# Performance work log

Measured on AMD Instinct MI355X. Metric: run time of the kernel, lower is better.

Reference implementation:

```python
import jax, jax.numpy as jnp
import numpy as np


def setup_inputs() -> dict:
    key = jax.random.key(0)
    ks = jax.random.split(key, 7)
    N, D, H1, H2, M = 16384, 2048, 512, 32, 2048
    return {
        "x": jax.random.normal(ks[0], (N, D), dtype=jnp.float32),
        "W1": jax.random.normal(ks[1], (H1, D), dtype=jnp.float32) * (1.0 / np.sqrt(D)),
        "b1": jax.random.normal(ks[2], (H1,), dtype=jnp.float32) * 0.01,
        "W2": jax.random.normal(ks[3], (H2, H1), dtype=jnp.float32) * (1.0 / np.sqrt(H1)),
        "b2": jax.random.normal(ks[4], (H2,), dtype=jnp.float32) * 0.01,
        "a_memory": jax.random.normal(ks[5], (M, H2), dtype=jnp.float32),
        "n_memory": jax.random.normal(ks[6], (M, H2), dtype=jnp.float32),
    }


def reference(x, W1, b1, W2, b2, a_memory, n_memory):
    # MLP per forward(): linear -> relu -> (dropout p=0) -> linear -> (dropout p=0)
    h = jax.nn.relu(x @ W1.T + b1)          # [N, 512]
    feat = h @ W2.T + b2                     # [N, 32] (no ReLU in forward path)
    inv_d = 1.0 / feat.shape[1]
    # caption_score(mem, f) = max_j mean(mem_j * f) = max_j (mem_j . f) / 32
    a_score = jnp.max(feat @ a_memory.T, axis=1) * inv_d  # [N]
    n_score = jnp.max(feat @ n_memory.T, axis=1) * inv_d  # [N]
    return jax.nn.sigmoid(a_score - n_score)
```

## Files before the change

### kernel.cpp

```cpp
#include <hip/hip_runtime.h>
#include <hip/hip_bf16.h>

typedef __attribute__((ext_vector_type(8))) __bf16 bf16x8;
typedef __attribute__((ext_vector_type(4))) float f32x4;

#define NROWS 16384
#define DIM   2048
#define NH1   512
#define NH2   32
#define MMEM  2048
#define BK    32
#define NT    (DIM / BK)

#define W1O ((size_t)0)
#define W2O ((size_t)2097152)
#define AMO ((size_t)2129920)
#define NMO ((size_t)2260992)
#define HO  ((size_t)2392064)

__device__ __forceinline__ f32x4 mfma16(bf16x8 a, bf16x8 b, f32x4 c) {
    return __builtin_amdgcn_mfma_f32_16x16x32_bf16(a, b, c, 0, 0, 0);
}

__device__ __forceinline__ void gload_lds16(const void* g, void* l) {
    __builtin_amdgcn_global_load_lds(
        (const __attribute__((address_space(1))) void*)g,
        (__attribute__((address_space(3))) void*)l, 16, 0, 0);
}

__device__ __forceinline__ bf16x8 cvt8(f32x4 a, f32x4 b) {
    bf16x8 o;
    o[0] = (__bf16)a[0]; o[1] = (__bf16)a[1]; o[2] = (__bf16)a[2]; o[3] = (__bf16)a[3];
    o[4] = (__bf16)b[0]; o[5] = (__bf16)b[1]; o[6] = (__bf16)b[2]; o[7] = (__bf16)b[3];
    return o;
}

struct bf4 { __bf16 a, b, c, d; };

__global__ void cvt_all_kernel(const float* __restrict__ w1f, __bf16* __restrict__ w1b,
                               const float* __restrict__ w2f, __bf16* __restrict__ w2b,
                               const float* __restrict__ amf, __bf16* __restrict__ amb,
                               const float* __restrict__ nmf, __bf16* __restrict__ nmb) {
    const int g = blockIdx.x * blockDim.x + threadIdx.x;
    const int T = gridDim.x * blockDim.x;
    for (int i = g; i < (NH1 * DIM) / 4; i += T) {
        const float4 v = *reinterpret_cast<const float4*>(w1f + i * 4);
        *reinterpret_cast<bf4*>(w1b + i * 4) = { (__bf16)v.x, (__bf16)v.y, (__bf16)v.z, (__bf16)v.w };
    }
    for (int i = g; i < (NH2 * NH1) / 4; i += T) {
        const float4 v = *reinterpret_cast<const float4*>(w2f + i * 4);
        *reinterpret_cast<bf4*>(w2b + i * 4) = { (__bf16)v.x, (__bf16)v.y, (__bf16)v.z, (__bf16)v.w };
    }
    for (int i = g; i < (MMEM * NH2) / 4; i += T) {
        const float4 v = *reinterpret_cast<const float4*>(amf + i * 4);
        *reinterpret_cast<bf4*>(amb + i * 4) = { (__bf16)v.x, (__bf16)v.y, (__bf16)v.z, (__bf16)v.w };
    }
    for (int i = g; i < (MMEM * NH2) / 4; i += T) {
        const float4 v = *reinterpret_cast<const float4*>(nmf + i * 4);
        *reinterpret_cast<bf4*>(nmb + i * 4) = { (__bf16)v.x, (__bf16)v.y, (__bf16)v.z, (__bf16)v.w };
    }
}

__global__ __launch_bounds__(256, 2) void gemm1_kernel(
    const float*  __restrict__ Xf,
    const __bf16* __restrict__ W1,
    const float*  __restrict__ b1,
    __bf16* __restrict__ Hout)
{
    __shared__ float  As[3][128 * BK];
    __shared__ __bf16 Bs[3][128 * BK];
    const int tid  = threadIdx.x;
    const int lane = tid & 63;
    const int wave = tid >> 6;
    const int b = blockIdx.x;
    const int orig = (b & 7) * 64 + (b >> 3);
    const int bn = orig & 3;
    const int bm = orig >> 2;
    const size_t brow = (size_t)bm * 128;
    const int bcol = bn * 128;
    const int wr = wave >> 1, wc = wave & 1;

    f32x4 acc[4][4];
#pragma unroll
    for (int m = 0; m < 4; ++m)
#pragma unroll
        for (int n = 0; n < 4; ++n) acc[m][n] = (f32x4){0.f, 0.f, 0.f, 0.f};

    const int aRowT = tid >> 3;
    const int cA    = (tid & 7) ^ (aRowT & 7);
    const float* aSrcBase = Xf + (brow + aRowT) * (size_t)DIM + cA * 4;
    const int bl  = (tid & 7) ^ ((tid >> 3) & 7);
    const int bh  = bl >> 2;
    const int bc  = bl & 3;
    const __bf16* bSrcBase = W1 + (size_t)(bcol + 2 * (tid >> 3) + bh) * DIM + bc * 8;

#define STAGE(T, BI)                                                          \
    {                                                                         \
        const int k0_ = (T) * BK;                                             \
        _Pragma("unroll")                                                     \
        for (int q = 0; q < 4; ++q)                                           \
            gload_lds16(aSrcBase + (size_t)q * 32 * DIM + k0_,                \
                        (char*)As[BI] + q * 4096 + tid * 16);                 \
        _Pragma("unroll")                                                     \
        for (int q = 0; q < 2; ++q)                                           \
            gload_lds16(bSrcBase + (size_t)q * 64 * DIM + k0_,                \
                        (char*)Bs[BI] + q * 4096 + tid * 16);                 \
    }

    const int l15 = lane & 15;
    const int kc  = lane >> 4;
    const int l7  = lane & 7;
    const int rABase = wr * 64 + l15;
    const int aSlot0 = ((2 * kc)     ^ l7) << 4;
    const int aSlot1 = ((2 * kc + 1) ^ l7) << 4;
    const int bByteBase = (wc * 32 + (l15 >> 1)) * 128 +
                          ((((l15 & 1) * 4 + kc) ^ (l15 >> 1)) << 4);

#define COMPUTE(BI)                                                           \
    {                                                                         \
        const char* Ac = (const char*)As[BI];                                 \
        const char* Bc = (const char*)Bs[BI];                                 \
        bf16x8 av[4], bv[4];                                                  \
        _Pragma("unroll")                                                     \
        for (int m = 0; m < 4; ++m) {                                         \
            const int rowB = (rABase + m * 16) * 128;                         \
            f32x4 lo = *(const f32x4*)(Ac + rowB + aSlot0);                   \
            f32x4 hi = *(const f32x4*)(Ac + rowB + aSlot1);                   \
            av[m] = cvt8(lo, hi);                                             \
        }                                                                     \
        _Pragma("unroll")                                                     \
        for (int n = 0; n < 4; ++n)                                           \
            bv[n] = *(const bf16x8*)(Bc + bByteBase + n * 1024);              \
        __builtin_amdgcn_s_setprio(1);                                        \
        _Pragma("unroll")                                                     \
        for (int m = 0; m < 4; ++m)                                           \
            _Pragma("unroll")                                                 \
            for (int n = 0; n < 4; ++n)                                       \
                acc[m][n] = mfma16(av[m], bv[n], acc[m][n]);                  \
        __builtin_amdgcn_s_setprio(0);                                        \
    }

    STAGE(0, 0);
    STAGE(1, 1);

    for (int t = 0; t < NT - 2; ++t) {
        const int bi = t % 3;
        asm volatile("s_waitcnt vmcnt(6)" ::: "memory");
        __builtin_amdgcn_s_barrier();
        __builtin_amdgcn_sched_barrier(0);
        COMPUTE(bi);
        __builtin_amdgcn_sched_barrier(0);
        const int bnx = (t + 2) % 3;
        STAGE(t + 2, bnx);
    }
    {
        asm volatile("s_waitcnt vmcnt(6)" ::: "memory");
        __builtin_amdgcn_s_barrier();
        __builtin_amdgcn_sched_barrier(0);
        COMPUTE((NT - 2) % 3);
        asm volatile("s_waitcnt vmcnt(0)" ::: "memory");
        __builtin_amdgcn_s_barrier();
        __builtin_amdgcn_sched_barrier(0);
        COMPUTE((NT - 1) % 3);
    }
#undef STAGE
#undef COMPUTE

#pragma unroll
    for (int n = 0; n < 4; ++n) {
        const int gcol = bcol + wc * 64 + n * 16 + l15;
        const float bias = b1[gcol];
#pragma unroll
        for (int m = 0; m < 4; ++m) {
            const size_t grow0 = brow + wr * 64 + m * 16 + kc * 4;
#pragma unroll
            for (int r = 0; r < 4; ++r) {
                float v = acc[m][n][r] + bias;
                v = v > 0.f ? v : 0.f;
                Hout[(grow0 + r) * NH1 + gcol] = (__bf16)v;
            }
        }
    }
}

__global__ __launch_bounds__(512) void tail_kernel(
    const __bf16* __restrict__ Hin,
    const __bf16* __restrict__ W2b,
    const float*  __restrict__ b2,
    const __bf16* __restrict__ Am,
    const __bf16* __restrict__ Nm,
    float* __restrict__ out)
{
    __shared__ __bf16 featLds[64 * 32];
    __shared__ float aMaxLds[2][64];
    __shared__ float nMaxLds[2][64];
    const int tid  = threadIdx.x;
    const int lane = tid & 63;
    const int wave = tid >> 6;
    const int rowBase = blockIdx.x * 64;
    const int l15 = lane & 15;
    const int kc  = lane >> 4;
    const int rgrp  = (wave & 3) * 16;
    const int jHalf = wave >> 2;

    if (wave < 4) {
        f32x4 acc0 = {0.f,0.f,0.f,0.f}, acc1 = {0.f,0.f,0.f,0.f};
        const size_t hrow = (size_t)(rowBase + rgrp + l15) * NH1;
#pragma unroll
        for (int kk = 0; kk < 16; ++kk) {
            bf16x8 a  = *(const bf16x8*)(Hin + hrow + kk * 32 + kc * 8);
            bf16x8 w0 = *(const bf16x8*)(W2b + (size_t)l15 * NH1 + kk * 32 + kc * 8);
            bf16x8 w1 = *(const bf16x8*)(W2b + (size_t)(16 + l15) * NH1 + kk * 32 + kc * 8);
            acc0 = mfma16(a, w0, acc0);
            acc1 = mfma16(a, w1, acc1);
        }
        const float bias0 = b2[l15], bias1 = b2[16 + l15];
#pragma unroll
        for (int r = 0; r < 4; ++r) {
            const int lr = rgrp + kc * 4 + r;
            featLds[lr * 32 + l15]      = (__bf16)(acc0[r] + bias0);
            featLds[lr * 32 + 16 + l15] = (__bf16)(acc1[r] + bias1);
        }
    }
    __syncthreads();

    const bf16x8 af = *(const bf16x8*)&featLds[(rgrp + l15) * 32 + kc * 8];

    float rmaxA[4], rmaxN[4];
#pragma unroll
    for (int r = 0; r < 4; ++r) { rmaxA[r] = -1e30f; rmaxN[r] = -1e30f; }
    const f32x4 zero = {0.f,0.f,0.f,0.f};
    const int jBase = jHalf * (MMEM / 2);
#pragma unroll 2
    for (int jt = 0; jt < (MMEM / 2) / 16; jt += 4) {
        bf16x8 ba[4], bb[4];
#pragma unroll
        for (int u = 0; u < 4; ++u) {
            const size_t off = (size_t)(jBase + (jt + u) * 16 + l15) * NH2 + kc * 8;
            ba[u] = *(const bf16x8*)(Am + off);
            bb[u] = *(const bf16x8*)(Nm + off);
        }
#pragma unroll
        for (int u = 0; u < 4; ++u) {
            f32x4 sa = mfma16(af, ba[u], zero);
            f32x4 sn = mfma16(af, bb[u], zero);
#pragma unroll
            for (int r = 0; r < 4; ++r) {
                rmaxA[r] = fmaxf(rmaxA[r], sa[r]);
                rmaxN[r] = fmaxf(rmaxN[r], sn[r]);
            }
        }
    }
#pragma unroll
    for (int off = 1; off < 16; off <<= 1) {
#pragma unroll
        for (int r = 0; r < 4; ++r) {
            rmaxA[r] = fmaxf(rmaxA[r], __shfl_xor(rmaxA[r], off, 64));
            rmaxN[r] = fmaxf(rmaxN[r], __shfl_xor(rmaxN[r], off, 64));
        }
    }
    if (l15 == 0) {
#pragma unroll
        for (int r = 0; r < 4; ++r) {
            const int row = rgrp + kc * 4 + r;
            aMaxLds[jHalf][row] = rmaxA[r];
            nMaxLds[jHalf][row] = rmaxN[r];
        }
    }
    __syncthreads();
    if (tid < 64) {
        const float ma = fmaxf(aMaxLds[0][tid], aMaxLds[1][tid]);
        const float mn = fmaxf(nMaxLds[0][tid], nMaxLds[1][tid]);
        const float d = (ma - mn) * (1.0f / 32.0f);
        out[rowBase + tid] = 1.0f / (1.0f + __expf(-d));
    }
}

extern "C" void kernel_launch(void* const* d_in, const int* in_sizes, int n_in,
                              void* d_out, int out_size, void* d_ws, size_t ws_size,
                              hipStream_t stream) {
    (void)in_sizes; (void)n_in; (void)out_size; (void)ws_size;
    const float* x  = (const float*)d_in[0];
    const float* W1 = (const float*)d_in[1];
    const float* b1 = (const float*)d_in[2];
    const float* W2 = (const float*)d_in[3];
    const float* b2 = (const float*)d_in[4];
    const float* am = (const float*)d_in[5];
    const float* nm = (const float*)d_in[6];
    float* out = (float*)d_out;
    char* ws = (char*)d_ws;
    __bf16* w1b = (__bf16*)(ws + W1O);
    __bf16* w2b = (__bf16*)(ws + W2O);
    __bf16* amb = (__bf16*)(ws + AMO);
    __bf16* nmb = (__bf16*)(ws + NMO);
    __bf16* hb  = (__bf16*)(ws + HO);

    cvt_all_kernel<<<dim3(512), dim3(256), 0, stream>>>(W1, w1b, W2, w2b, am, amb, nm, nmb);
    gemm1_kernel<<<dim3((NROWS / 128) * (NH1 / 128)), dim3(256), 0, stream>>>(x, w1b, b1, hb);
    tail_kernel<<<dim3(NROWS / 64), dim3(512), 0, stream>>>(hb, w2b, b2, amb, nmb, out);
}
```

Baseline: 81.95 us.

## Convert X tile to bf16 in registers before LDS staging in gemm1

```diff
diff --git a/kernel.cpp b/kernel.cpp
--- a/kernel.cpp
+++ b/kernel.cpp
@@ -67,7 +67,7 @@
     const float*  __restrict__ b1,
     __bf16* __restrict__ Hout)
 {
-    __shared__ float  As[3][128 * BK];
+    __shared__ __bf16 As[3][64 * 64];
     __shared__ __bf16 Bs[3][128 * BK];
     const int tid  = threadIdx.x;
     const int lane = tid & 63;
@@ -86,35 +86,45 @@
 #pragma unroll
         for (int n = 0; n < 4; ++n) acc[m][n] = (f32x4){0.f, 0.f, 0.f, 0.f};
 
-    const int aRowT = tid >> 3;
-    const int cA    = (tid & 7) ^ (aRowT & 7);
-    const float* aSrcBase = Xf + (brow + aRowT) * (size_t)DIM + cA * 4;
+    const int aR  = tid >> 2;
+    const int aH  = (tid >> 1) & 1;
+    const int aC0 = (tid & 1) * 2;
+    const float* aSrc = Xf + (brow + 2 * aR + aH) * (size_t)DIM + aC0 * 8;
+    const int aW0 = aR * 128 + (((aH * 4 + aC0)     ^ (aR & 7)) << 4);
+    const int aW1 = aR * 128 + (((aH * 4 + aC0 + 1) ^ (aR & 7)) << 4);
+
     const int bl  = (tid & 7) ^ ((tid >> 3) & 7);
     const int bh  = bl >> 2;
     const int bc  = bl & 3;
     const __bf16* bSrcBase = W1 + (size_t)(bcol + 2 * (tid >> 3) + bh) * DIM + bc * 8;
 
-#define STAGE(T, BI)                                                          \
+#define STAGE_B(T, BI)                                                        \
     {                                                                         \
         const int k0_ = (T) * BK;                                             \
-        _Pragma("unroll")                                                     \
-        for (int q = 0; q < 4; ++q)                                           \
-            gload_lds16(aSrcBase + (size_t)q * 32 * DIM + k0_,                \
-                        (char*)As[BI] + q * 4096 + tid * 16);                 \
         _Pragma("unroll")                                                     \
         for (int q = 0; q < 2; ++q)                                           \
             gload_lds16(bSrcBase + (size_t)q * 64 * DIM + k0_,                \
                         (char*)Bs[BI] + q * 4096 + tid * 16);                 \
     }
 
+#define LOAD_PA(T)                                                            \
+    {                                                                         \
+        const float* qs_ = aSrc + (size_t)(T) * BK;                           \
+        _Pragma("unroll")                                                     \
+        for (int i = 0; i < 4; ++i) pa[i] = *(const f32x4*)(qs_ + i * 4);     \
+    }
+
+#define WRITE_A(BI)                                                           \
+    {                                                                         \
+        *(bf16x8*)((char*)As[BI] + aW0) = cvt8(pa[0], pa[1]);                 \
+        *(bf16x8*)((char*)As[BI] + aW1) = cvt8(pa[2], pa[3]);                 \
+    }
+
     const int l15 = lane & 15;
     const int kc  = lane >> 4;
-    const int l7  = lane & 7;
-    const int rABase = wr * 64 + l15;
-    const int aSlot0 = ((2 * kc)     ^ l7) << 4;
-    const int aSlot1 = ((2 * kc + 1) ^ l7) << 4;
-    const int bByteBase = (wc * 32 + (l15 >> 1)) * 128 +
-                          ((((l15 & 1) * 4 + kc) ^ (l15 >> 1)) << 4);
+    const int slotB = ((((l15 & 1) * 4 + kc) ^ (l15 >> 1)) << 4);
+    const int aByteBase = (wr * 32 + (l15 >> 1)) * 128 + slotB;
+    const int bByteBase = (wc * 32 + (l15 >> 1)) * 128 + slotB;
 
 #define COMPUTE(BI)                                                           \
     {                                                                         \
@@ -122,12 +132,8 @@
         const char* Bc = (const char*)Bs[BI];                                 \
         bf16x8 av[4], bv[4];                                                  \
         _Pragma("unroll")                                                     \
-        for (int m = 0; m < 4; ++m) {                                         \
-            const int rowB = (rABase + m * 16) * 128;                         \
-            f32x4 lo = *(const f32x4*)(Ac + rowB + aSlot0);                   \
-            f32x4 hi = *(const f32x4*)(Ac + rowB + aSlot1);                   \
-            av[m] = cvt8(lo, hi);                                             \
-        }                                                                     \
+        for (int m = 0; m < 4; ++m)                                           \
+            av[m] = *(const bf16x8*)(Ac + aByteBase + m * 1024);              \
         _Pragma("unroll")                                                     \
         for (int n = 0; n < 4; ++n)                                           \
             bv[n] = *(const bf16x8*)(Bc + bByteBase + n * 1024);              \
@@ -140,30 +146,43 @@
         __builtin_amdgcn_s_setprio(0);                                        \
     }
 
-    STAGE(0, 0);
-    STAGE(1, 1);
+    f32x4 pa[4];
+
+    STAGE_B(0, 0);
+    LOAD_PA(0);
+    WRITE_A(0);
+    STAGE_B(1, 1);
+    LOAD_PA(1);
 
     for (int t = 0; t < NT - 2; ++t) {
-        const int bi = t % 3;
-        asm volatile("s_waitcnt vmcnt(6)" ::: "memory");
+        asm volatile("s_waitcnt vmcnt(6) lgkmcnt(0)" ::: "memory");
         __builtin_amdgcn_s_barrier();
         __builtin_amdgcn_sched_barrier(0);
-        COMPUTE(bi);
-        __builtin_amdgcn_sched_barrier(0);
-        const int bnx = (t + 2) % 3;
-        STAGE(t + 2, bnx);
+        STAGE_B(t + 2, (t + 2) % 3);
+        __builtin_amdgcn_sched_barrier(0);
+        WRITE_A((t + 1) % 3);
+        __builtin_amdgcn_sched_barrier(0);
+        LOAD_PA(t + 2);
+        __builtin_amdgcn_sched_barrier(0);
+        COMPUTE(t % 3);
     }
     {
-        asm volatile("s_waitcnt vmcnt(6)" ::: "memory");
+        asm volatile("s_waitcnt vmcnt(6) lgkmcnt(0)" ::: "memory");
         __builtin_amdgcn_s_barrier();
         __builtin_amdgcn_sched_barrier(0);
+        WRITE_A((NT - 1) % 3);
+        __builtin_amdgcn_sched_barrier(0);
         COMPUTE((NT - 2) % 3);
-        asm volatile("s_waitcnt vmcnt(0)" ::: "memory");
+    }
+    {
+        asm volatile("s_waitcnt vmcnt(0) lgkmcnt(0)" ::: "memory");
         __builtin_amdgcn_s_barrier();
         __builtin_amdgcn_sched_barrier(0);
         COMPUTE((NT - 1) % 3);
     }
-#undef STAGE
+#undef STAGE_B
+#undef LOAD_PA
+#undef WRITE_A
 #undef COMPUTE
 
 #pragma unroll
```

After: 92.19 us. 12.5% more time.
